# Optimization experiments

Measured on AMD Instinct MI355X. Metric: run time of the kernel, lower is better.

## Reference

```python
import jax, jax.numpy as jnp
import numpy as np

BS, SEQ, DIM, NH = 2, 2048, 2048, 16
HD = DIM // NH  # 128


def setup_inputs() -> dict:
    key = jax.random.key(0)
    ks = jax.random.split(key, 6)
    x = jax.random.normal(ks[0], (BS, SEQ, DIM), dtype=jnp.float32)
    # rotary frequencies, theta=10000 as in LLaMA
    inv_freq = 1.0 / (10000.0 ** (jnp.arange(0, HD, 2, dtype=jnp.float32) / HD))  # [HD/2]
    t = jnp.arange(SEQ, dtype=jnp.float32)
    freqs = jnp.outer(t, inv_freq)  # [SEQ, HD/2]
    freqs_cos = jnp.cos(freqs)
    freqs_sin = jnp.sin(freqs)
    # additive causal mask [1,1,S,S]
    causal = jnp.tril(jnp.ones((SEQ, SEQ), dtype=bool))
    mask = jnp.where(causal, 0.0, -1e9).astype(jnp.float32)[None, None]
    scale = 0.02
    wq = jax.random.normal(ks[1], (DIM, DIM), dtype=jnp.float32) * scale
    wk = jax.random.normal(ks[2], (DIM, DIM), dtype=jnp.float32) * scale
    wv = jax.random.normal(ks[3], (DIM, DIM), dtype=jnp.float32) * scale
    wo = jax.random.normal(ks[4], (DIM, DIM), dtype=jnp.float32) * scale
    return {"x": x, "freqs_cos": freqs_cos, "freqs_sin": freqs_sin, "mask": mask,
            "wq": wq, "wk": wk, "wv": wv, "wo": wo}


def _apply_rope(t, cos, sin):
    # t: [b,s,h,hd]; cos/sin: [s,hd/2]
    tr = t.reshape(*t.shape[:-1], HD // 2, 2)
    tre, tim = tr[..., 0], tr[..., 1]
    c = cos[None, :, None, :]
    s = sin[None, :, None, :]
    out_re = tre * c - tim * s
    out_im = tre * s + tim * c
    return jnp.stack([out_re, out_im], axis=-1).reshape(t.shape)


def reference(x, freqs_cos, freqs_sin, mask, wq, wk, wv, wo):
    bs, seq, _ = x.shape
    q = (x @ wq).reshape(bs, seq, NH, HD)
    k = (x @ wk).reshape(bs, seq, NH, HD)
    v = (x @ wv).reshape(bs, seq, NH, HD)
    q = _apply_rope(q, freqs_cos, freqs_sin)
    k = _apply_rope(k, freqs_cos, freqs_sin)
    # [b,h,s,s]
    scores = jnp.einsum("bqhd,bkhd->bhqk", q, k) / np.sqrt(HD).astype(np.float32)
    scores = scores + mask
    probs = jax.nn.softmax(scores, axis=-1)
    out = jnp.einsum("bhqk,bkhd->bqhd", probs, v).reshape(bs, seq, DIM)
    return out @ wo
```

## Files before the change

### kernel.cpp

```cpp
#include <hip/hip_runtime.h>
#include <hip/hip_bf16.h>
#include <stdint.h>
#include <stddef.h>

#define SEQ 2048
#define DIM 2048
#define NH 16
#define HD 128
#define BSZ 2
#define MTOT (BSZ*SEQ)
#define KDIM DIM

typedef __bf16 bf16;
typedef __attribute__((ext_vector_type(4))) __bf16 bf16x4;
typedef __attribute__((ext_vector_type(8))) __bf16 bf16x8;
typedef __attribute__((ext_vector_type(4))) float f32x4;

#define MFMA16(a,b,c) __builtin_amdgcn_mfma_f32_16x16x32_bf16((a),(b),(c),0,0,0)

__device__ __forceinline__ void glds16(const void* g, void* l) {
  __builtin_amdgcn_global_load_lds((__attribute__((address_space(1))) void*)(g),
                                   (__attribute__((address_space(3))) void*)(l),
                                   16, 0, 0);
}

__device__ __forceinline__ f32x4 f4zero() { f32x4 v = {0.f, 0.f, 0.f, 0.f}; return v; }

__device__ __forceinline__ uint32_t bpack(float a, float b) {
  uint16_t au = __builtin_bit_cast(uint16_t, (bf16)a);
  uint16_t bu = __builtin_bit_cast(uint16_t, (bf16)b);
  return (uint32_t)au | ((uint32_t)bu << 16);
}

__global__ void cast_x_bf16(const float* __restrict__ in, bf16* __restrict__ out) {
  size_t i = (size_t)blockIdx.x * blockDim.x + threadIdx.x;
  float4 v = ((const float4*)in)[i];
  bf16x4 ov;
  ov.x = (bf16)v.x; ov.y = (bf16)v.y; ov.z = (bf16)v.z; ov.w = (bf16)v.w;
  ((bf16x4*)out)[i] = ov;
}

__global__ void transpose_w(const float* __restrict__ W, bf16* __restrict__ WT) {
  __shared__ float tile[64][65];
  const int bk = blockIdx.x, bn = blockIdx.y;
  const int tid = threadIdx.x;
  const int tc = tid & 15, tr = tid >> 4;
#pragma unroll
  for (int p = 0; p < 4; ++p) {
    int k = tr + p * 16;
    float4 v = *(const float4*)(W + (size_t)(bk * 64 + k) * DIM + bn * 64 + tc * 4);
    tile[k][tc * 4 + 0] = v.x;
    tile[k][tc * 4 + 1] = v.y;
    tile[k][tc * 4 + 2] = v.z;
    tile[k][tc * 4 + 3] = v.w;
  }
  __syncthreads();
#pragma unroll
  for (int p = 0; p < 4; ++p) {
    int n = tr + p * 16;
    bf16x4 ov;
    ov.x = (bf16)tile[tc * 4 + 0][n];
    ov.y = (bf16)tile[tc * 4 + 1][n];
    ov.z = (bf16)tile[tc * 4 + 2][n];
    ov.w = (bf16)tile[tc * 4 + 3][n];
    *(bf16x4*)(WT + (size_t)(bn * 64 + n) * DIM + bk * 64 + tc * 4) = ov;
  }
}

template<int EPI>
__global__ __launch_bounds__(256, 2)
void gemm_bf16(const bf16* __restrict__ A, const bf16* __restrict__ BT,
               void* __restrict__ Cout,
               const float* __restrict__ cosT, const float* __restrict__ sinT)
{
  __shared__ __align__(16) bf16 As[2][128 * 32];
  __shared__ __align__(16) bf16 Bs[2][128 * 32];
  const int tid = threadIdx.x;
  const int lane = tid & 63;
  const int w = tid >> 6;
  const int l15 = lane & 15, h4 = lane >> 4;
  const int wr = w >> 1, wc = w & 1;
  const int bn = blockIdx.x, bm = blockIdx.y;
  const int rowA0 = bm * 128, colB0 = bn * 128;

  f32x4 acc[4][4];
#pragma unroll
  for (int m = 0; m < 4; ++m)
#pragma unroll
    for (int n = 0; n < 4; ++n) acc[m][n] = f4zero();

  const uint8_t* Abytes = (const uint8_t*)A;
  const uint8_t* Bbytes = (const uint8_t*)BT;

  auto stage = [&](int buf, int t) {
    const int k0b = t * 64;
#pragma unroll
    for (int j = 0; j < 2; ++j) {
      int chunk = w * 128 + j * 64 + lane;
      int row = chunk >> 2, c = chunk & 3;
      int jj = (c * 16) ^ (((row >> 1) & 3) << 4);
      glds16(Abytes + (size_t)(rowA0 + row) * (KDIM * 2) + k0b + jj,
             (uint8_t*)&As[buf][0] + (w * 128 + j * 64) * 16);
      glds16(Bbytes + (size_t)(colB0 + row) * (KDIM * 2) + k0b + jj,
             (uint8_t*)&Bs[buf][0] + (w * 128 + j * 64) * 16);
    }
  };

  stage(0, 0);
  __syncthreads();

  const int NT = KDIM / 32;
  for (int t = 0; t < NT; ++t) {
    int cur = t & 1;
    if (t + 1 < NT) stage(cur ^ 1, t + 1);
    const uint8_t* Ab = (const uint8_t*)&As[cur][0];
    const uint8_t* Bb = (const uint8_t*)&Bs[cur][0];
    bf16x8 aF[4], bF[4];
#pragma unroll
    for (int m = 0; m < 4; ++m) {
      int row = wr * 64 + m * 16 + l15;
      int off = row * 64 + ((h4 * 16) ^ (((row >> 1) & 3) << 4));
      aF[m] = *(const bf16x8*)(Ab + off);
    }
#pragma unroll
    for (int n = 0; n < 4; ++n) {
      int row = wc * 64 + n * 16 + l15;
      int off = row * 64 + ((h4 * 16) ^ (((row >> 1) & 3) << 4));
      bF[n] = *(const bf16x8*)(Bb + off);
    }
#pragma unroll
    for (int m = 0; m < 4; ++m)
#pragma unroll
      for (int n = 0; n < 4; ++n)
        acc[m][n] = MFMA16(aF[m], bF[n], acc[m][n]);
    __syncthreads();
  }

  const int row0 = rowA0 + wr * 64, col0 = colB0 + wc * 64;
#pragma unroll
  for (int m = 0; m < 4; ++m) {
#pragma unroll
    for (int n = 0; n < 4; ++n) {
#pragma unroll
      for (int r = 0; r < 4; ++r) {
        int row = row0 + m * 16 + h4 * 4 + r;
        int col = col0 + n * 16 + l15;
        float v = acc[m][n][r];
        if constexpr (EPI == 0) {
          ((float*)Cout)[(size_t)row * DIM + col] = v;
        } else if constexpr (EPI == 1) {
          float v2 = __shfl_xor(v, 1);
          int s = row & (SEQ - 1);
          int jidx = (col & (HD - 1)) >> 1;
          float c = cosT[s * (HD / 2) + jidx];
          float sn = sinT[s * (HD / 2) + jidx];
          float o = (col & 1) ? fmaf(v2, sn, v * c) : fmaf(v, c, -(v2 * sn));
          ((bf16*)Cout)[(size_t)row * DIM + col] = (bf16)o;
        } else {
          int hh = col >> 7, d = col & (HD - 1);
          int b = row >> 11, s = row & (SEQ - 1);
          ((bf16*)Cout)[((size_t)(b * NH + hh) * HD + d) * SEQ + s] = (bf16)v;
        }
      }
    }
  }
}

__global__ __launch_bounds__(256, 2)
void flash_attn(const bf16* __restrict__ Q, const bf16* __restrict__ Kg,
                const bf16* __restrict__ VT, bf16* __restrict__ O)
{
  __shared__ __align__(16) bf16 Ks[2][64 * 128];
  __shared__ __align__(16) bf16 Vs[2][128 * 64];

  const int pr = blockIdx.x, h = blockIdx.y, b = blockIdx.z;
  const int tid = threadIdx.x, lane = tid & 63, w = tid >> 6;
  const int l15 = lane & 15, h4 = lane >> 4;
  const bool hhalf = ((h4 >> 1) & 1) != 0;

  const float scale = 0.08838834764831845f;
  const uint8_t* kgb = (const uint8_t*)Kg + ((size_t)(b * SEQ) * DIM + h * HD) * 2;
  const uint8_t* vgb = (const uint8_t*)VT + ((size_t)(b * NH + h) * HD * SEQ) * 2;

  auto stageKV = [&](int buf, int t) {
    const uint8_t* ksrc = kgb + (size_t)t * 64 * (DIM * 2);
    const uint8_t* vsrc = vgb + (size_t)t * 64 * 2;
#pragma unroll
    for (int j = 0; j < 4; ++j) {
      int chunk = w * 256 + j * 64 + lane;
      int key = chunk >> 4, ck = chunk & 15;
      int jk = (ck * 16) ^ ((key & 7) << 4);
      glds16(ksrc + (size_t)key * (DIM * 2) + jk,
             (uint8_t*)&Ks[buf][0] + (w * 256 + j * 64) * 16);
      int d = chunk >> 3, cv = chunk & 7;
      int jv = (cv * 16) ^ ((d & 7) << 4);
      glds16(vsrc + (size_t)d * (SEQ * 2) + jv,
             (uint8_t*)&Vs[buf][0] + (w * 256 + j * 64) * 16);
    }
  };

#pragma unroll 1
  for (int qsel = 0; qsel < 2; ++qsel) {
    const int qt = qsel ? (SEQ / 64 - 1 - pr) : pr;
    const int q0 = qt * 64;
    const int qrow = q0 + w * 16 + l15;

    const bf16* qbase = Q + ((size_t)(b * SEQ + qrow)) * DIM + h * HD;
    bf16x8 aQ[4];
#pragma unroll
    for (int kk = 0; kk < 4; ++kk)
      aQ[kk] = *(const bf16x8*)(qbase + kk * 32 + h4 * 8);

    f32x4 o[8];
#pragma unroll
    for (int i = 0; i < 8; ++i) o[i] = f4zero();
    float mrun = -1e30f, lrun = 0.0f;

    stageKV(0, 0);
    __syncthreads();

#pragma unroll 1
    for (int t = 0; t <= qt; ++t) {
      const int cur = t & 1;
      if (t < qt) stageKV(cur ^ 1, t + 1);

      f32x4 S[4];
      __builtin_amdgcn_s_setprio(1);
#pragma unroll
      for (int kb = 0; kb < 4; ++kb) {
        f32x4 a = f4zero();
        int key = kb * 16 + l15;
        int swz = (key & 7) << 4;
#pragma unroll
        for (int kk = 0; kk < 4; ++kk) {
          bf16x8 aK = *(const bf16x8*)((const uint8_t*)&Ks[cur][0] + key * 256 +
                                       (((kk * 32 + h4 * 8) * 2) ^ swz));
          a = MFMA16(aK, aQ[kk], a);
        }
        S[kb] = a;
      }
      __builtin_amdgcn_s_setprio(0);

      if (t == qt) {
#pragma unroll
        for (int kb = 0; kb < 4; ++kb)
#pragma unroll
          for (int r = 0; r < 4; ++r) {
            int key = q0 + kb * 16 + h4 * 4 + r;
            float sv = S[kb][r] * scale;
            S[kb][r] = (key > qrow) ? -1e9f : sv;
          }
      } else {
#pragma unroll
        for (int kb = 0; kb < 4; ++kb)
#pragma unroll
          for (int r = 0; r < 4; ++r) S[kb][r] *= scale;
      }

      float pmax = S[0][0];
#pragma unroll
      for (int kb = 0; kb < 4; ++kb)
#pragma unroll
        for (int r = 0; r < 4; ++r) pmax = fmaxf(pmax, S[kb][r]);
      pmax = fmaxf(pmax, __shfl_xor(pmax, 16));
      pmax = fmaxf(pmax, __shfl_xor(pmax, 32));
      float mnew = fmaxf(mrun, pmax);
      float corr = __expf(mrun - mnew);
      float p[4][4];
      float psum = 0.f;
#pragma unroll
      for (int kb = 0; kb < 4; ++kb)
#pragma unroll
        for (int r = 0; r < 4; ++r) {
          float pv = __expf(S[kb][r] - mnew);
          p[kb][r] = pv;
          psum += pv;
        }
      psum += __shfl_xor(psum, 16);
      psum += __shfl_xor(psum, 32);
      lrun = lrun * corr + psum;
      mrun = mnew;
#pragma unroll
      for (int i = 0; i < 8; ++i) o[i] *= corr;

      uint32_t pk[4][2];
#pragma unroll
      for (int kb = 0; kb < 4; ++kb) {
        pk[kb][0] = bpack(p[kb][0], p[kb][1]);
        pk[kb][1] = bpack(p[kb][2], p[kb][3]);
      }

      bf16x8 pB[2];
#pragma unroll
      for (int kb2 = 0; kb2 < 2; ++kb2) {
        uint32_t s0a = hhalf ? pk[kb2 * 2 + 1][0] : pk[kb2 * 2][0];
        uint32_t s0b = hhalf ? pk[kb2 * 2 + 1][1] : pk[kb2 * 2][1];
        uint32_t s1a = hhalf ? pk[kb2 * 2][0] : pk[kb2 * 2 + 1][0];
        uint32_t s1b = hhalf ? pk[kb2 * 2][1] : pk[kb2 * 2 + 1][1];
        uint32_t e16a = __shfl_xor(s0a, 16), e16b = __shfl_xor(s0b, 16);
        uint32_t e32a = __shfl_xor(s1a, 32), e32b = __shfl_xor(s1b, 32);
        uint32_t e48a = __shfl_xor(s1a, 48), e48b = __shfl_xor(s1b, 48);
        uint32_t lo0 = (h4 == 0) ? s0a : (h4 == 1) ? e48a : (h4 == 2) ? e32a : e16a;
        uint32_t lo1 = (h4 == 0) ? s0b : (h4 == 1) ? e48b : (h4 == 2) ? e32b : e16b;
        uint32_t hi0 = (h4 == 0) ? e16a : (h4 == 1) ? e32a : (h4 == 2) ? e48a : s0a;
        uint32_t hi1 = (h4 == 0) ? e16b : (h4 == 1) ? e32b : (h4 == 2) ? e48b : s0b;
        uint4 u = make_uint4(lo0, lo1, hi0, hi1);
        pB[kb2] = __builtin_bit_cast(bf16x8, u);
      }

      __builtin_amdgcn_s_setprio(1);
#pragma unroll
      for (int db = 0; db < 8; ++db) {
        int drow = db * 16 + l15;
        int swz = (drow & 7) << 4;
#pragma unroll
        for (int kb2 = 0; kb2 < 2; ++kb2) {
          bf16x8 aV = *(const bf16x8*)((const uint8_t*)&Vs[cur][0] + drow * 128 +
                                       (((kb2 * 32 + h4 * 8) * 2) ^ swz));
          o[db] = MFMA16(aV, pB[kb2], o[db]);
        }
      }
      __builtin_amdgcn_s_setprio(0);

      __syncthreads();
    }

    float inv = 1.0f / lrun;
    bf16* obase = O + ((size_t)(b * SEQ + qrow)) * DIM + h * HD;
#pragma unroll
    for (int db = 0; db < 8; ++db) {
      uint32_t w0 = bpack(o[db][0] * inv, o[db][1] * inv);
      uint32_t w1 = bpack(o[db][2] * inv, o[db][3] * inv);
      uint2 st = make_uint2(w0, w1);
      *(uint2*)(obase + db * 16 + h4 * 4) = st;
    }
  }
}

extern "C" void kernel_launch(void* const* d_in, const int* in_sizes, int n_in,
                              void* d_out, int out_size, void* d_ws, size_t ws_size,
                              hipStream_t stream)
{
  const float* x    = (const float*)d_in[0];
  const float* fcos = (const float*)d_in[1];
  const float* fsin = (const float*)d_in[2];
  const float* wq   = (const float*)d_in[4];
  const float* wk   = (const float*)d_in[5];
  const float* wv   = (const float*)d_in[6];
  const float* wo   = (const float*)d_in[7];

  uint8_t* ws = (uint8_t*)d_ws;
  const size_t SZ_XB = (size_t)MTOT * DIM * 2;
  const size_t SZ_WT = (size_t)DIM * DIM * 2;

  bf16* xb    = (bf16*)(ws);
  bf16* wqT   = (bf16*)(ws + SZ_XB);
  bf16* wkT   = (bf16*)(ws + SZ_XB + 1 * SZ_WT);
  bf16* wvT   = (bf16*)(ws + SZ_XB + 2 * SZ_WT);
  bf16* woT   = (bf16*)(ws + SZ_XB + 3 * SZ_WT);
  bf16* qb    = (bf16*)(ws + SZ_XB + 4 * SZ_WT);
  bf16* kb    = (bf16*)(ws + 2 * SZ_XB + 4 * SZ_WT);
  bf16* vT    = (bf16*)(ws + 3 * SZ_XB + 4 * SZ_WT);
  bf16* attnb = xb;

  cast_x_bf16<<<(MTOT * DIM) / (256 * 4), 256, 0, stream>>>(x, xb);
  dim3 tg(DIM / 64, DIM / 64);
  transpose_w<<<tg, 256, 0, stream>>>(wq, wqT);
  transpose_w<<<tg, 256, 0, stream>>>(wk, wkT);
  transpose_w<<<tg, 256, 0, stream>>>(wv, wvT);
  transpose_w<<<tg, 256, 0, stream>>>(wo, woT);

  dim3 gg(DIM / 128, MTOT / 128);
  gemm_bf16<1><<<gg, 256, 0, stream>>>(xb, wqT, qb, fcos, fsin);
  gemm_bf16<1><<<gg, 256, 0, stream>>>(xb, wkT, kb, fcos, fsin);
  gemm_bf16<2><<<gg, 256, 0, stream>>>(xb, wvT, vT, nullptr, nullptr);

  flash_attn<<<dim3(SEQ / 128, NH, BSZ), 256, 0, stream>>>(qb, kb, vT, attnb);

  gemm_bf16<0><<<gg, 256, 0, stream>>>(attnb, woT, (float*)d_out, nullptr, nullptr);
}
```

Before: 440.3 us.

## Fuse QKV projections into one larger-tile GEMM and remap blocks for locality

Replaces the three separate Q/K/V projection GEMMs with a single launch over a concatenated weight (wqT, wkT, wvT laid out contiguously) and picks the RoPE or V-transpose epilogue per column segment. The GEMM moves to 256x128 tiles with 512 threads, a K step of 128, a two-deep glds prefetch using explicit vmcnt waits, and an XOR-swizzled 98KB dynamic LDS buffer. Block indices are remapped across groups of 8, likely to spread neighbouring tiles across XCDs and improve L2 reuse, and flash attention gets a similar 1D grid remap. The goal is fewer launches and higher MFMA utilisation. The cost is higher LDS and register pressure, which may limit occupancy.

```diff
diff --git a/kernel.cpp b/kernel.cpp
--- a/kernel.cpp
+++ b/kernel.cpp
@@ -9,7 +9,8 @@
 #define HD 128
 #define BSZ 2
 #define MTOT (BSZ*SEQ)
-#define KDIM DIM
+#define KDIM 2048
+#define NT_K (KDIM/64)
 
 typedef __bf16 bf16;
 typedef __attribute__((ext_vector_type(4))) __bf16 bf16x4;
@@ -67,21 +68,48 @@
   }
 }
 
-template<int EPI>
-__global__ __launch_bounds__(256, 2)
-void gemm_bf16(const bf16* __restrict__ A, const bf16* __restrict__ BT,
-               void* __restrict__ Cout,
-               const float* __restrict__ cosT, const float* __restrict__ sinT)
+template<int MODE>
+__global__ __launch_bounds__(512, 2)
+void gemm8(const bf16* __restrict__ A, const bf16* __restrict__ BT,
+           float* __restrict__ out0,
+           bf16* __restrict__ qb, bf16* __restrict__ kbuf, bf16* __restrict__ vT,
+           const float* __restrict__ cosT, const float* __restrict__ sinT)
 {
-  __shared__ __align__(16) bf16 As[2][128 * 32];
-  __shared__ __align__(16) bf16 Bs[2][128 * 32];
+  extern __shared__ uint8_t smem[];
   const int tid = threadIdx.x;
-  const int lane = tid & 63;
-  const int w = tid >> 6;
+  const int lane = tid & 63, w = tid >> 6;
   const int l15 = lane & 15, h4 = lane >> 4;
-  const int wr = w >> 1, wc = w & 1;
-  const int bn = blockIdx.x, bm = blockIdx.y;
-  const int rowA0 = bm * 128, colB0 = bn * 128;
+  const int wr = w & 3, wc = w >> 2;
+
+  const int f = blockIdx.x;
+  const int cpx = gridDim.x >> 3;
+  const int swz = (f & 7) * cpx + (f >> 3);
+  const int bm = swz & 15;
+  const int bn = swz >> 4;
+
+  const size_t strideB = (size_t)KDIM * 2;
+  const uint8_t* Ab = (const uint8_t*)A + (size_t)(bm * 256) * strideB;
+  const uint8_t* Bb = (const uint8_t*)BT + (size_t)(bn * 128) * strideB;
+
+  auto stage = [&](int buf, int t) {
+    uint8_t* la = smem + buf * 49152;
+    uint8_t* lb = la + 32768;
+    const int kb0 = t * 128;
+#pragma unroll
+    for (int i = 0; i < 4; ++i) {
+      int chunk = i * 512 + tid;
+      int row = chunk >> 3, c = chunk & 7;
+      int cs = c ^ (row & 7);
+      glds16(Ab + (size_t)row * strideB + kb0 + cs * 16, la + chunk * 16);
+    }
+#pragma unroll
+    for (int i = 0; i < 2; ++i) {
+      int chunk = i * 512 + tid;
+      int row = chunk >> 3, c = chunk & 7;
+      int cs = c ^ (row & 7);
+      glds16(Bb + (size_t)row * strideB + kb0 + cs * 16, lb + chunk * 16);
+    }
+  };
 
   f32x4 acc[4][4];
 #pragma unroll
@@ -89,54 +117,51 @@
 #pragma unroll
     for (int n = 0; n < 4; ++n) acc[m][n] = f4zero();
 
-  const uint8_t* Abytes = (const uint8_t*)A;
-  const uint8_t* Bbytes = (const uint8_t*)BT;
-
-  auto stage = [&](int buf, int t) {
-    const int k0b = t * 64;
-#pragma unroll
-    for (int j = 0; j < 2; ++j) {
-      int chunk = w * 128 + j * 64 + lane;
-      int row = chunk >> 2, c = chunk & 3;
-      int jj = (c * 16) ^ (((row >> 1) & 3) << 4);
-      glds16(Abytes + (size_t)(rowA0 + row) * (KDIM * 2) + k0b + jj,
-             (uint8_t*)&As[buf][0] + (w * 128 + j * 64) * 16);
-      glds16(Bbytes + (size_t)(colB0 + row) * (KDIM * 2) + k0b + jj,
-             (uint8_t*)&Bs[buf][0] + (w * 128 + j * 64) * 16);
-    }
-  };
-
   stage(0, 0);
-  __syncthreads();
-
-  const int NT = KDIM / 32;
-  for (int t = 0; t < NT; ++t) {
-    int cur = t & 1;
-    if (t + 1 < NT) stage(cur ^ 1, t + 1);
-    const uint8_t* Ab = (const uint8_t*)&As[cur][0];
-    const uint8_t* Bb = (const uint8_t*)&Bs[cur][0];
-    bf16x8 aF[4], bF[4];
+  stage(1, 1);
+
+#pragma unroll 1
+  for (int t = 0; t < NT_K; ++t) {
+    if (t < NT_K - 1) { asm volatile("s_waitcnt vmcnt(6)" ::: "memory"); }
+    else              { asm volatile("s_waitcnt vmcnt(0)" ::: "memory"); }
+    __builtin_amdgcn_s_barrier();
+    asm volatile("" ::: "memory");
+
+    const uint8_t* la = smem + (t & 1) * 49152;
+    const uint8_t* lb = la + 32768;
+    bf16x8 aF[4][2], bF[4][2];
 #pragma unroll
     for (int m = 0; m < 4; ++m) {
       int row = wr * 64 + m * 16 + l15;
-      int off = row * 64 + ((h4 * 16) ^ (((row >> 1) & 3) << 4));
-      aF[m] = *(const bf16x8*)(Ab + off);
+#pragma unroll
+      for (int ks = 0; ks < 2; ++ks)
+        aF[m][ks] = *(const bf16x8*)(la + row * 128 + (((ks * 4 + h4) ^ (row & 7)) * 16));
     }
 #pragma unroll
     for (int n = 0; n < 4; ++n) {
       int row = wc * 64 + n * 16 + l15;
-      int off = row * 64 + ((h4 * 16) ^ (((row >> 1) & 3) << 4));
-      bF[n] = *(const bf16x8*)(Bb + off);
-    }
-#pragma unroll
-    for (int m = 0; m < 4; ++m)
-#pragma unroll
-      for (int n = 0; n < 4; ++n)
-        acc[m][n] = MFMA16(aF[m], bF[n], acc[m][n]);
-    __syncthreads();
+#pragma unroll
+      for (int ks = 0; ks < 2; ++ks)
+        bF[n][ks] = *(const bf16x8*)(lb + row * 128 + (((ks * 4 + h4) ^ (row & 7)) * 16));
+    }
+    __builtin_amdgcn_s_setprio(1);
+#pragma unroll
+    for (int ks = 0; ks < 2; ++ks)
+#pragma unroll
+      for (int m = 0; m < 4; ++m)
+#pragma unroll
+        for (int n = 0; n < 4; ++n)
+          acc[m][n] = MFMA16(aF[m][ks], bF[n][ks], acc[m][n]);
+    __builtin_amdgcn_s_setprio(0);
+
+    asm volatile("" ::: "memory");
+    __builtin_amdgcn_s_barrier();
+    asm volatile("" ::: "memory");
+    if (t + 2 < NT_K) stage(t & 1, t + 2);
   }
 
-  const int row0 = rowA0 + wr * 64, col0 = colB0 + wc * 64;
+  const int row0 = bm * 256 + wr * 64;
+  const int col0 = bn * 128 + wc * 64;
 #pragma unroll
   for (int m = 0; m < 4; ++m) {
 #pragma unroll
@@ -146,20 +171,25 @@
         int row = row0 + m * 16 + h4 * 4 + r;
         int col = col0 + n * 16 + l15;
         float v = acc[m][n][r];
-        if constexpr (EPI == 0) {
-          ((float*)Cout)[(size_t)row * DIM + col] = v;
-        } else if constexpr (EPI == 1) {
-          float v2 = __shfl_xor(v, 1);
-          int s = row & (SEQ - 1);
-          int jidx = (col & (HD - 1)) >> 1;
-          float c = cosT[s * (HD / 2) + jidx];
-          float sn = sinT[s * (HD / 2) + jidx];
-          float o = (col & 1) ? fmaf(v2, sn, v * c) : fmaf(v, c, -(v2 * sn));
-          ((bf16*)Cout)[(size_t)row * DIM + col] = (bf16)o;
+        if constexpr (MODE == 0) {
+          out0[(size_t)row * DIM + col] = v;
         } else {
-          int hh = col >> 7, d = col & (HD - 1);
-          int b = row >> 11, s = row & (SEQ - 1);
-          ((bf16*)Cout)[((size_t)(b * NH + hh) * HD + d) * SEQ + s] = (bf16)v;
+          int seg = col >> 11;
+          int ccol = col & (DIM - 1);
+          if (seg < 2) {
+            float v2 = __shfl_xor(v, 1);
+            int s = row & (SEQ - 1);
+            int jidx = (ccol & (HD - 1)) >> 1;
+            float c = cosT[s * (HD / 2) + jidx];
+            float sn = sinT[s * (HD / 2) + jidx];
+            float o = (col & 1) ? fmaf(v2, sn, v * c) : fmaf(v, c, -(v2 * sn));
+            bf16* dst = (seg == 0) ? qb : kbuf;
+            dst[(size_t)row * DIM + ccol] = (bf16)o;
+          } else {
+            int hh = ccol >> 7, d = ccol & (HD - 1);
+            int bb = row >> 11, s = row & (SEQ - 1);
+            vT[((size_t)(bb * NH + hh) * HD + d) * SEQ + s] = (bf16)v;
+          }
         }
       }
     }
@@ -173,7 +203,12 @@
   __shared__ __align__(16) bf16 Ks[2][64 * 128];
   __shared__ __align__(16) bf16 Vs[2][128 * 64];
 
-  const int pr = blockIdx.x, h = blockIdx.y, b = blockIdx.z;
+  const int fidx = blockIdx.x;
+  const int xr = fidx & 7, inner = fidx >> 3;
+  const int pr = inner & 15;
+  const int g = xr + 8 * (inner >> 4);
+  const int h = g & 15, b = g >> 4;
+
   const int tid = threadIdx.x, lane = tid & 63, w = tid >> 6;
   const int l15 = lane & 15, h4 = lane >> 4;
   const bool hhalf = ((h4 >> 1) & 1) != 0;
@@ -230,11 +265,11 @@
       for (int kb = 0; kb < 4; ++kb) {
         f32x4 a = f4zero();
         int key = kb * 16 + l15;
-        int swz = (key & 7) << 4;
+        int swzk = (key & 7) << 4;
 #pragma unroll
         for (int kk = 0; kk < 4; ++kk) {
           bf16x8 aK = *(const bf16x8*)((const uint8_t*)&Ks[cur][0] + key * 256 +
-                                       (((kk * 32 + h4 * 8) * 2) ^ swz));
+                                       (((kk * 32 + h4 * 8) * 2) ^ swzk));
           a = MFMA16(aK, aQ[kk], a);
         }
         S[kb] = a;
@@ -312,11 +347,11 @@
 #pragma unroll
       for (int db = 0; db < 8; ++db) {
         int drow = db * 16 + l15;
-        int swz = (drow & 7) << 4;
+        int swzv = (drow & 7) << 4;
 #pragma unroll
         for (int kb2 = 0; kb2 < 2; ++kb2) {
           bf16x8 aV = *(const bf16x8*)((const uint8_t*)&Vs[cur][0] + drow * 128 +
-                                       (((kb2 * 32 + h4 * 8) * 2) ^ swz));
+                                       (((kb2 * 32 + h4 * 8) * 2) ^ swzv));
           o[db] = MFMA16(aV, pB[kb2], o[db]);
         }
       }
@@ -363,6 +398,11 @@
   bf16* vT    = (bf16*)(ws + 3 * SZ_XB + 4 * SZ_WT);
   bf16* attnb = xb;
 
+  hipFuncSetAttribute((const void*)gemm8<1>,
+                      hipFuncAttributeMaxDynamicSharedMemorySize, 98304);
+  hipFuncSetAttribute((const void*)gemm8<0>,
+                      hipFuncAttributeMaxDynamicSharedMemorySize, 98304);
+
   cast_x_bf16<<<(MTOT * DIM) / (256 * 4), 256, 0, stream>>>(x, xb);
   dim3 tg(DIM / 64, DIM / 64);
   transpose_w<<<tg, 256, 0, stream>>>(wq, wqT);
@@ -370,12 +410,10 @@
   transpose_w<<<tg, 256, 0, stream>>>(wv, wvT);
   transpose_w<<<tg, 256, 0, stream>>>(wo, woT);
 
-  dim3 gg(DIM / 128, MTOT / 128);
-  gemm_bf16<1><<<gg, 256, 0, stream>>>(xb, wqT, qb, fcos, fsin);
-  gemm_bf16<1><<<gg, 256, 0, stream>>>(xb, wkT, kb, fcos, fsin);
-  gemm_bf16<2><<<gg, 256, 0, stream>>>(xb, wvT, vT, nullptr, nullptr);
-
-  flash_attn<<<dim3(SEQ / 128, NH, BSZ), 256, 0, stream>>>(qb, kb, vT, attnb);
-
-  gemm_bf16<0><<<gg, 256, 0, stream>>>(attnb, woT, (float*)d_out, nullptr, nullptr);
-}
+  gemm8<1><<<768, 512, 98304, stream>>>(xb, wqT, nullptr, qb, kb, vT, fcos, fsin);
+
+  flash_attn<<<512, 256, 0, stream>>>(qb, kb, vT, attnb);
+
+  gemm8<0><<<256, 512, 98304, stream>>>(attnb, woT, (float*)d_out,
+                                        nullptr, nullptr, nullptr, nullptr, nullptr);
+}
```

Measured after the change: 434.6 us. No clear change (-1.3%).
